# Optimization experiments

Measured on AMD Instinct MI355X. Metric: run time of the kernel, lower is better.

Reference implementation:

```python
import jax, jax.numpy as jnp
import numpy as np

C_EM, H_EM, C_A = 256, 8, 32
S, R = 1024, 256
LN_EPS = 1e-5
MASK_BIAS = 1e9


def setup_inputs() -> dict:
    key = jax.random.key(0)
    ks = jax.random.split(key, 8)
    sc = 0.02
    m = jax.random.normal(ks[0], (S, R, C_EM), jnp.float32)
    # binary column mask (float mask in the original; int here so it is a constant)
    mask = (jax.random.uniform(ks[1], (S, R)) < 0.9).astype(jnp.int32)
    return {
        "m": m,
        "ln_g": jnp.ones((C_EM,), jnp.float32),
        "ln_b": jnp.zeros((C_EM,), jnp.float32),
        "w_q": jax.random.normal(ks[2], (C_EM, H_EM, C_A), jnp.float32) * sc,
        "w_k": jax.random.normal(ks[3], (C_EM, C_A), jnp.float32) * sc,
        "w_v": jax.random.normal(ks[4], (C_EM, C_A), jnp.float32) * sc,
        "w_g": jax.random.normal(ks[5], (C_EM, H_EM, C_A), jnp.float32) * sc,
        "b_g": jnp.zeros((H_EM, C_A), jnp.float32),
        "w_o": jax.random.normal(ks[6], (H_EM, C_A, C_EM), jnp.float32) * sc,
        "b_o": jnp.zeros((C_EM,), jnp.float32),
        "mask": mask,
    }


def reference(m, ln_g, ln_b, w_q, w_k, w_v, w_g, b_g, w_o, b_o, mask):
    maskf = mask.astype(m.dtype)  # [s, r]
    # LayerNorm over c_em (biased variance, eps=1e-5, torch default)
    mu = jnp.mean(m, axis=-1, keepdims=True)
    var = jnp.mean((m - mu) ** 2, axis=-1, keepdims=True)
    x = (m - mu) * jax.lax.rsqrt(var + LN_EPS) * ln_g + ln_b  # [s, r, c]
    # masked mean-pool over s -> per-column query
    q_pool = jnp.sum(x * maskf[..., None], axis=-3) / (jnp.sum(maskf, axis=-2)[..., None] + 1e-10)  # [r, c]
    Q = jnp.einsum('rc,chd->rhd', q_pool, w_q) * (1.0 / np.sqrt(C_A))  # [r, h, d]
    K = jnp.einsum('src,cd->srd', x, w_k)  # [s, r, d]
    V = jnp.einsum('src,cd->srd', x, w_v)  # [s, r, d]
    G = jax.nn.sigmoid(jnp.einsum('src,chd->srhd', x, w_g) + b_g)  # [s, r, h, d]
    bias = (maskf - 1.0) * MASK_BIAS  # [s, r]
    logits = jnp.einsum('rhd,srd->srh', Q, K) + bias[..., None]  # [s, r, h]
    A = jax.nn.softmax(logits, axis=-3)  # softmax over s
    O = jnp.einsum('srh,srd->rhd', A, V)  # [r, h, d]
    out = jnp.einsum('srhd,hdc->src', O[None, :, :, :] * G, w_o) + b_o  # [s, r, c]
    return out
```

## Files before the change

### kernel.cpp

```cpp
#include <hip/hip_runtime.h>
#include <math.h>

#define S_DIM 1024
#define R_DIM 256
#define C_DIM 256
#define SCALE 0.17677669529663687f

typedef short bf16x8 __attribute__((ext_vector_type(8)));
typedef float f32x4 __attribute__((ext_vector_type(4)));

__device__ __forceinline__ float wred(float v) {
#pragma unroll
  for (int m = 32; m >= 1; m >>= 1) v += __shfl_xor(v, m, 64);
  return v;
}

__device__ __forceinline__ short f2bf(float f) {
  union { float f; unsigned u; } v;
  v.f = f;
  unsigned r = v.u + 0x7fffu + ((v.u >> 16) & 1u);
  return (short)(r >> 16);
}

__device__ __forceinline__ float bf2f(short s) {
  union { unsigned u; float f; } v;
  v.u = ((unsigned)(unsigned short)s) << 16;
  return v.f;
}

__device__ __forceinline__ float fast_sigmoid_mul(float o, float gl) {
  return o * __builtin_amdgcn_rcpf(1.f + __expf(-gl));
}

__global__ __launch_bounds__(256)
void k0_prep(const float* __restrict__ w_g, const float* __restrict__ w_o,
             const float* __restrict__ w_k, const float* __restrict__ w_v,
             short* __restrict__ wgB, short* __restrict__ woB,
             short* __restrict__ wkvB) {
  const int id = blockIdx.x * 256 + threadIdx.x;
  if (id < 16384) {
    const int which = id >> 13;
    const int s = id & 8191;
    const int n = s & 255, g = (s >> 8) & 3, kb = s >> 10;
    const float* W = which ? w_o : w_g;
    short* Out = which ? woB : wgB;
#pragma unroll
    for (int j = 0; j < 8; ++j)
      Out[(((size_t)kb * 256 + n) * 4 + g) * 8 + j] =
          f2bf(W[(size_t)(kb * 32 + g * 8 + j) * 256 + n]);
  } else {
    const int s = id - 16384;
    const int n = s & 63, g = (s >> 6) & 3, kb = s >> 8;
    const float* W = (n < 32) ? w_k : w_v;
    const int nn = n & 31;
#pragma unroll
    for (int j = 0; j < 8; ++j)
      wkvB[(((size_t)kb * 64 + n) * 4 + g) * 8 + j] =
          f2bf(W[(size_t)(kb * 32 + g * 8 + j) * 32 + nn]);
  }
}

__global__ __launch_bounds__(256, 3)
void k1_ln_kv(const float* __restrict__ mIn, const float* __restrict__ ln_g,
              const float* __restrict__ ln_b, const short* __restrict__ wkvB,
              const int* __restrict__ mask,
              float* __restrict__ mu_ws, float* __restrict__ rs_ws,
              short* __restrict__ Kt, short* __restrict__ Vt,
              float* __restrict__ pool_ws) {
  __shared__ __align__(16) short A_lds[2048 * 8];
  __shared__ float mask_s[64];
  __shared__ float4 poolp[4][64];
  const int r  = blockIdx.y;
  const int s0 = blockIdx.x * 64;
  const int t  = threadIdx.x;

  if (t < 64) mask_s[t] = mask[(s0 + t) * R_DIM + r] ? 1.f : 0.f;

  {
    const int rw = t >> 2;
    const int q  = t & 3;
    const size_t p = (size_t)(s0 + rw) * R_DIM + r;
    const float* src = mIn + p * C_DIM + q * 64;
    float4 xv[16];
    float sum = 0.f, ssq = 0.f;
#pragma unroll
    for (int i = 0; i < 16; ++i) {
      xv[i] = *(const float4*)(src + i * 4);
      sum += xv[i].x + xv[i].y + xv[i].z + xv[i].w;
      ssq += xv[i].x * xv[i].x + xv[i].y * xv[i].y + xv[i].z * xv[i].z +
             xv[i].w * xv[i].w;
    }
    sum += __shfl_xor(sum, 1, 64); ssq += __shfl_xor(ssq, 1, 64);
    sum += __shfl_xor(sum, 2, 64); ssq += __shfl_xor(ssq, 2, 64);
    const float mu = sum * (1.f / 256.f);
    const float var = ssq * (1.f / 256.f) - mu * mu;
    const float rs = rsqrtf(var + 1e-5f);
    if (q == 0) { mu_ws[p] = mu; rs_ws[p] = rs; }

    const int gw = rw >> 4;
    const int lf0 = rw & 15;
#pragma unroll
    for (int kh = 0; kh < 2; ++kh) {
      const int kb = 2 * q + kh;
#pragma unroll
      for (int g = 0; g < 4; ++g) {
        const int lidx = kh * 32 + g * 8;
        const float4 a0 = xv[lidx >> 2], a1 = xv[(lidx >> 2) + 1];
        const float4 g0 = *(const float4*)(ln_g + kb * 32 + g * 8);
        const float4 g1 = *(const float4*)(ln_g + kb * 32 + g * 8 + 4);
        const float4 b0 = *(const float4*)(ln_b + kb * 32 + g * 8);
        const float4 b1 = *(const float4*)(ln_b + kb * 32 + g * 8 + 4);
        bf16x8 f;
        f[0] = f2bf((a0.x - mu) * rs * g0.x + b0.x);
        f[1] = f2bf((a0.y - mu) * rs * g0.y + b0.y);
        f[2] = f2bf((a0.z - mu) * rs * g0.z + b0.z);
        f[3] = f2bf((a0.w - mu) * rs * g0.w + b0.w);
        f[4] = f2bf((a1.x - mu) * rs * g1.x + b1.x);
        f[5] = f2bf((a1.y - mu) * rs * g1.y + b1.y);
        f[6] = f2bf((a1.z - mu) * rs * g1.z + b1.z);
        f[7] = f2bf((a1.w - mu) * rs * g1.w + b1.w);
        int byte = (((gw * 8 + kb) * 64 + lf0 + g * 16) << 4) ^ (((kb >> 1) & 3) << 5);
        *(bf16x8*)((char*)A_lds + byte) = f;
      }
    }
  }
  __syncthreads();

  {
    const int w = t >> 6, l = t & 63;
    const int lm = l & 15, g = l >> 4;
    f32x4 acc[4];
#pragma unroll
    for (int ni = 0; ni < 4; ++ni) acc[ni] = (f32x4){0.f, 0.f, 0.f, 0.f};
#pragma unroll
    for (int kb = 0; kb < 8; ++kb) {
      const int byte = (((w * 8 + kb) * 64 + l) << 4) ^ (((kb >> 1) & 3) << 5);
      const bf16x8 a = *(const bf16x8*)((char*)A_lds + byte);
      bf16x8 bfr[4];
#pragma unroll
      for (int ni = 0; ni < 4; ++ni)
        bfr[ni] = *(const bf16x8*)(wkvB + (((size_t)kb * 64 + lm + ni * 16) * 4 + g) * 8);
#pragma unroll
      for (int ni = 0; ni < 4; ++ni)
        acc[ni] = __builtin_amdgcn_mfma_f32_16x16x32_bf16(a, bfr[ni], acc[ni], 0, 0, 0);
    }
#pragma unroll
    for (int ni = 0; ni < 4; ++ni) {
      const int col = lm + ni * 16;
      short* Out = (col < 32) ? Kt : Vt;
      const int cc = col & 31;
#pragma unroll
      for (int reg = 0; reg < 4; ++reg) {
        const int s = s0 + w * 16 + g * 4 + reg;
        Out[((size_t)r * 1024 + s) * 32 + cc] = f2bf(acc[ni][reg]);
      }
    }
  }

  {
    const int lc = t & 63;
    const int wq = t >> 6;
    const int kb = lc >> 3, g2 = (lc >> 1) & 3, bh = (lc & 1) * 4;
    float4 ps = make_float4(0.f, 0.f, 0.f, 0.f);
    for (int i = 0; i < 16; ++i) {
      const int rloc = (i + lc) & 15;
      const int byte =
          ((((wq * 8 + kb) * 64 + rloc + g2 * 16) << 4) + bh * 2) ^ (((kb >> 1) & 3) << 5);
      const short4 xb = *(const short4*)((char*)A_lds + byte);
      const float mk = mask_s[wq * 16 + rloc];
      ps.x += mk * bf2f(xb.x);
      ps.y += mk * bf2f(xb.y);
      ps.z += mk * bf2f(xb.z);
      ps.w += mk * bf2f(xb.w);
    }
    poolp[wq][lc] = ps;
  }
  __syncthreads();
  if (t < 64) {
    const float4 a = poolp[0][t], b = poolp[1][t], c = poolp[2][t], d = poolp[3][t];
    atomicAdd(&pool_ws[r * C_DIM + t * 4 + 0], a.x + b.x + c.x + d.x);
    atomicAdd(&pool_ws[r * C_DIM + t * 4 + 1], a.y + b.y + c.y + d.y);
    atomicAdd(&pool_ws[r * C_DIM + t * 4 + 2], a.z + b.z + c.z + d.z);
    atomicAdd(&pool_ws[r * C_DIM + t * 4 + 3], a.w + b.w + c.w + d.w);
  }
}

__global__ __launch_bounds__(256, 2)
void k2_q(const float* __restrict__ pool_ws, const int* __restrict__ mask,
          const float* __restrict__ w_q, float* __restrict__ Q_ws) {
  __shared__ float qp[256];
  __shared__ float wsum[4];
  const int r = blockIdx.x, t = threadIdx.x;
  int cnt = 0;
  for (int s = t; s < S_DIM; s += 256) cnt += mask[s * R_DIM + r];
  float cf = wred((float)cnt);
  if ((t & 63) == 0) wsum[t >> 6] = cf;
  __syncthreads();
  const float denom = wsum[0] + wsum[1] + wsum[2] + wsum[3] + 1e-10f;
  qp[t] = pool_ws[r * C_DIM + t] / denom;
  __syncthreads();
  float acc = 0.f;
  for (int c = 0; c < 256; ++c) acc += qp[c] * w_q[c * 256 + t];
  Q_ws[r * 256 + t] = acc * SCALE;
}

__global__ __launch_bounds__(256, 4)
void k3e_logits(const short* __restrict__ Kt, const float* __restrict__ Q_ws,
                const int* __restrict__ mask, float* __restrict__ E_ws,
                float* __restrict__ D_ws) {
  __shared__ float q[256];
  const int r = blockIdx.y, s0 = blockIdx.x * 64;
  const int t = threadIdx.x, w = t >> 6, l = t & 63;
  q[t] = Q_ws[r * 256 + t];
  __syncthreads();
  const int s = s0 + l;
  const short* kp = Kt + ((size_t)r * 1024 + s) * 32;
  bf16x8 kr[4];
#pragma unroll
  for (int i = 0; i < 4; ++i) kr[i] = *(const bf16x8*)(kp + i * 8);
  const int mk = mask[s * R_DIM + r];
  float e01[2];
#pragma unroll
  for (int hh = 0; hh < 2; ++hh) {
    const int h = 2 * w + hh;
    float a = 0.f;
#pragma unroll
    for (int i = 0; i < 4; ++i)
#pragma unroll
      for (int j = 0; j < 8; ++j)
        a += q[h * 32 + i * 8 + j] * bf2f(kr[i][j]);
    e01[hh] = mk ? __expf(a) : 0.f;
    E_ws[((size_t)r * 8 + h) * 1024 + s] = e01[hh];
  }
  const float d0 = wred(e01[0]);
  const float d1 = wred(e01[1]);
  if (l == 0) {
    atomicAdd(&D_ws[r * 8 + 2 * w + 0], d0);
    atomicAdd(&D_ws[r * 8 + 2 * w + 1], d1);
  }
}

__global__ __launch_bounds__(256, 4)
void k3b_av(const short* __restrict__ Vt, const float* __restrict__ E_ws,
            float* __restrict__ Npart) {
  __shared__ float A_s[8 * 256];
  __shared__ __align__(16) short V_s[256 * 32];
  const int ch = blockIdx.x, r = blockIdx.y;
  const int t = threadIdx.x;
  const int sb = ch * 256;
#pragma unroll
  for (int h = 0; h < 8; ++h)
    A_s[h * 256 + t] = E_ws[((size_t)r * 8 + h) * 1024 + sb + t];
  {
    const short* vp = Vt + ((size_t)r * 1024 + sb) * 32;
#pragma unroll
    for (int i = 0; i < 4; ++i) {
      const int u = i * 256 + t;
      *(bf16x8*)(V_s + u * 8) = *(const bf16x8*)(vp + u * 8);
    }
  }
  __syncthreads();
  const int h = t >> 5, d = t & 31;
  const float* ap = A_s + h * 256;
  float o = 0.f;
  for (int s4 = 0; s4 < 256; s4 += 4) {
    const float4 a4 = *(const float4*)(ap + s4);
    o += a4.x * bf2f(V_s[(s4 + 0) * 32 + d]);
    o += a4.y * bf2f(V_s[(s4 + 1) * 32 + d]);
    o += a4.z * bf2f(V_s[(s4 + 2) * 32 + d]);
    o += a4.w * bf2f(V_s[(s4 + 3) * 32 + d]);
  }
  Npart[(size_t)ch * 65536 + r * 256 + t] = o;
}

__global__ __launch_bounds__(256)
void k3c_norm(const float* __restrict__ Npart, const float* __restrict__ D_ws,
              float* __restrict__ O_ws) {
  const int r = blockIdx.x, t = threadIdx.x;
  const int idx = r * 256 + t;
  const float n = Npart[idx] + Npart[65536 + idx] + Npart[131072 + idx] +
                  Npart[196608 + idx];
  O_ws[idx] = n / (D_ws[r * 8 + (t >> 5)] + 1e-30f);
}

__global__ __launch_bounds__(256, 4)
void k4_mfma(const float* __restrict__ mIn, const float* __restrict__ ln_g,
             const float* __restrict__ ln_b, const float* __restrict__ mu_ws,
             const float* __restrict__ rs_ws, const short* __restrict__ wgB,
             const float* __restrict__ b_g, const float* __restrict__ O_ws,
             const short* __restrict__ woB, const float* __restrict__ b_o,
             float* __restrict__ out) {
  __shared__ __align__(16) short A_lds[2048 * 8];
  const int t = threadIdx.x;
  const int p0 = blockIdx.x * 64;
  const int r0 = p0 & 255;
  const int l = t & 63;
  const int w = t >> 6;
  const int lm = l & 15;
  const int g = l >> 4;

  {
    const int row = w * 16 + lm;
    const size_t p = (size_t)(p0 + row);
    const float mu = mu_ws[p], rs = rs_ws[p];
    const float* mrow = mIn + p * 256 + g * 8;
    const float* gp = ln_g + g * 8;
    const float* bp = ln_b + g * 8;
#pragma unroll
    for (int kb = 0; kb < 8; ++kb) {
      const float4 m0 = *(const float4*)(mrow + kb * 32);
      const float4 m1 = *(const float4*)(mrow + kb * 32 + 4);
      const float4 g0 = *(const float4*)(gp + kb * 32);
      const float4 g1 = *(const float4*)(gp + kb * 32 + 4);
      const float4 b0 = *(const float4*)(bp + kb * 32);
      const float4 b1 = *(const float4*)(bp + kb * 32 + 4);
      bf16x8 xf;
      xf[0] = f2bf((m0.x - mu) * rs * g0.x + b0.x);
      xf[1] = f2bf((m0.y - mu) * rs * g0.y + b0.y);
      xf[2] = f2bf((m0.z - mu) * rs * g0.z + b0.z);
      xf[3] = f2bf((m0.w - mu) * rs * g0.w + b0.w);
      xf[4] = f2bf((m1.x - mu) * rs * g1.x + b1.x);
      xf[5] = f2bf((m1.y - mu) * rs * g1.y + b1.y);
      xf[6] = f2bf((m1.z - mu) * rs * g1.z + b1.z);
      xf[7] = f2bf((m1.w - mu) * rs * g1.w + b1.w);
      *(bf16x8*)(A_lds + ((w * 8 + kb) * 64 + l) * 8) = xf;
    }
  }
  __syncthreads();

  const int col = w * 64 + lm;
  f32x4 acc[4][4];

#pragma unroll
  for (int ni = 0; ni < 4; ++ni) {
    const float bg = b_g[col + ni * 16];
#pragma unroll
    for (int mi = 0; mi < 4; ++mi) acc[mi][ni] = (f32x4){bg, bg, bg, bg};
  }
#pragma unroll
  for (int kb = 0; kb < 8; ++kb) {
    bf16x8 a[4], bb[4];
#pragma unroll
    for (int mi = 0; mi < 4; ++mi)
      a[mi] = *(const bf16x8*)(A_lds + ((mi * 8 + kb) * 64 + l) * 8);
#pragma unroll
    for (int ni = 0; ni < 4; ++ni)
      bb[ni] = *(const bf16x8*)(wgB + (((size_t)kb * 256 + col + ni * 16) * 4 + g) * 8);
#pragma unroll
    for (int mi = 0; mi < 4; ++mi)
#pragma unroll
      for (int ni = 0; ni < 4; ++ni)
        acc[mi][ni] = __builtin_amdgcn_mfma_f32_16x16x32_bf16(a[mi], bb[ni], acc[mi][ni], 0, 0, 0);
  }
  __syncthreads();

#pragma unroll
  for (int mi = 0; mi < 4; ++mi) {
#pragma unroll
    for (int ni = 0; ni < 4; ++ni) {
      const int c2 = col + ni * 16;
      const int kb2 = c2 >> 5, g2 = (c2 >> 3) & 3, b2 = c2 & 7;
#pragma unroll
      for (int reg = 0; reg < 4; ++reg) {
        const int row = mi * 16 + g * 4 + reg;
        const float o = O_ws[(r0 + row) * 256 + c2];
        const float tv = fast_sigmoid_mul(o, acc[mi][ni][reg]);
        const int u = (mi * 8 + kb2) * 64 + (g * 4 + reg) + g2 * 16;
        const int byte = ((u << 4) ^ (((u >> 4) & 3) << 4)) + b2 * 2;
        *(short*)((char*)A_lds + byte) = f2bf(tv);
      }
    }
  }
  __syncthreads();

#pragma unroll
  for (int ni = 0; ni < 4; ++ni) {
    const float bo = b_o[col + ni * 16];
#pragma unroll
    for (int mi = 0; mi < 4; ++mi) acc[mi][ni] = (f32x4){bo, bo, bo, bo};
  }
#pragma unroll
  for (int kb = 0; kb < 8; ++kb) {
    bf16x8 a[4], bb[4];
#pragma unroll
    for (int mi = 0; mi < 4; ++mi) {
      const int u = (mi * 8 + kb) * 64 + l;
      const int byte = (u << 4) ^ (g << 4);
      a[mi] = *(const bf16x8*)((char*)A_lds + byte);
    }
#pragma unroll
    for (int ni = 0; ni < 4; ++ni)
      bb[ni] = *(const bf16x8*)(woB + (((size_t)kb * 256 + col + ni * 16) * 4 + g) * 8);
#pragma unroll
    for (int mi = 0; mi < 4; ++mi)
#pragma unroll
      for (int ni = 0; ni < 4; ++ni)
        acc[mi][ni] = __builtin_amdgcn_mfma_f32_16x16x32_bf16(a[mi], bb[ni], acc[mi][ni], 0, 0, 0);
  }

#pragma unroll
  for (int mi = 0; mi < 4; ++mi)
#pragma unroll
    for (int ni = 0; ni < 4; ++ni)
#pragma unroll
      for (int reg = 0; reg < 4; ++reg) {
        const int row = mi * 16 + g * 4 + reg;
        out[(size_t)(p0 + row) * 256 + col + ni * 16] = acc[mi][ni][reg];
      }
}

extern "C" void kernel_launch(void* const* d_in, const int* in_sizes, int n_in,
                              void* d_out, int out_size, void* d_ws, size_t ws_size,
                              hipStream_t stream) {
  const float* mIn  = (const float*)d_in[0];
  const float* ln_g = (const float*)d_in[1];
  const float* ln_b = (const float*)d_in[2];
  const float* w_q  = (const float*)d_in[3];
  const float* w_k  = (const float*)d_in[4];
  const float* w_v  = (const float*)d_in[5];
  const float* w_g  = (const float*)d_in[6];
  const float* b_g  = (const float*)d_in[7];
  const float* w_o  = (const float*)d_in[8];
  const float* b_o  = (const float*)d_in[9];
  const int*   mask = (const int*)d_in[10];
  float* outp = (float*)d_out;

  float* ws = (float*)d_ws;
  const size_t NP = (size_t)S_DIM * R_DIM;
  float* mu_ws   = ws;
  float* rs_ws   = mu_ws + NP;
  short* Kt      = (short*)(rs_ws + NP);
  short* Vt      = Kt + (size_t)256 * 1024 * 32;
  float* pool_ws = (float*)(Vt + (size_t)256 * 1024 * 32);
  float* D_ws    = pool_ws + 65536;
  float* Q_ws    = D_ws + 2048;
  float* E_ws    = Q_ws + 65536;
  float* Npart   = E_ws + 2097152;
  float* O_ws    = Npart + 262144;
  short* wgB     = (short*)(O_ws + 65536);
  short* woB     = wgB + 65536;
  short* wkvB    = woB + 65536;

  hipMemsetAsync(pool_ws, 0, (65536 + 2048) * sizeof(float), stream);

  k0_prep<<<72, 256, 0, stream>>>(w_g, w_o, w_k, w_v, wgB, woB, wkvB);
  k1_ln_kv<<<dim3(S_DIM / 64, R_DIM), 256, 0, stream>>>(
      mIn, ln_g, ln_b, wkvB, mask, mu_ws, rs_ws, Kt, Vt, pool_ws);
  k2_q<<<R_DIM, 256, 0, stream>>>(pool_ws, mask, w_q, Q_ws);
  k3e_logits<<<dim3(S_DIM / 64, R_DIM), 256, 0, stream>>>(
      Kt, Q_ws, mask, E_ws, D_ws);
  k3b_av<<<dim3(4, R_DIM), 256, 0, stream>>>(Vt, E_ws, Npart);
  k3c_norm<<<R_DIM, 256, 0, stream>>>(Npart, D_ws, O_ws);
  k4_mfma<<<dim3(S_DIM * R_DIM / 64), 256, 0, stream>>>(
      mIn, ln_g, ln_b, mu_ws, rs_ws, wgB, b_g, O_ws, woB, b_o, outp);
}
```

Baseline: 368.3 us.

## Fuse logits and AV kernels, use packed bf16 conversion, raise k1 occupancy

Merges the logits/exp kernel and the attention-value kernel into one, so the exponentiated scores stay in shared memory and the 8 MB E workspace round trip is gone. Each block now also sums its exponentials for the softmax denominator. Separately, the scalar software bf16 rounding is replaced with the hardware v_cvt_pk_bf16_f32 pack instruction in both LN paths, and k1's launch bound goes from 3 to 4 waves. The fused kernel launches only 1024 blocks and keeps 32 K floats per thread in registers, which may cut parallelism. The higher occupancy target could cause register spills.

```diff
diff --git a/kernel.cpp b/kernel.cpp
--- a/kernel.cpp
+++ b/kernel.cpp
@@ -26,6 +26,22 @@
   union { unsigned u; float f; } v;
   v.u = ((unsigned)(unsigned short)s) << 16;
   return v.f;
+}
+
+__device__ __forceinline__ unsigned cvtpk(float lo, float hi) {
+  unsigned r;
+  asm volatile("v_cvt_pk_bf16_f32 %0, %1, %2" : "=v"(r) : "v"(lo), "v"(hi));
+  return r;
+}
+
+__device__ __forceinline__ bf16x8 pack8(float x0, float x1, float x2, float x3,
+                                        float x4, float x5, float x6, float x7) {
+  union { unsigned u[4]; bf16x8 v; } u_;
+  u_.u[0] = cvtpk(x0, x1);
+  u_.u[1] = cvtpk(x2, x3);
+  u_.u[2] = cvtpk(x4, x5);
+  u_.u[3] = cvtpk(x6, x7);
+  return u_.v;
 }
 
 __device__ __forceinline__ float fast_sigmoid_mul(float o, float gl) {
@@ -60,7 +76,7 @@
   }
 }
 
-__global__ __launch_bounds__(256, 3)
+__global__ __launch_bounds__(256, 4)
 void k1_ln_kv(const float* __restrict__ mIn, const float* __restrict__ ln_g,
               const float* __restrict__ ln_b, const short* __restrict__ wkvB,
               const int* __restrict__ mask,
@@ -110,15 +126,11 @@
         const float4 g1 = *(const float4*)(ln_g + kb * 32 + g * 8 + 4);
         const float4 b0 = *(const float4*)(ln_b + kb * 32 + g * 8);
         const float4 b1 = *(const float4*)(ln_b + kb * 32 + g * 8 + 4);
-        bf16x8 f;
-        f[0] = f2bf((a0.x - mu) * rs * g0.x + b0.x);
-        f[1] = f2bf((a0.y - mu) * rs * g0.y + b0.y);
-        f[2] = f2bf((a0.z - mu) * rs * g0.z + b0.z);
-        f[3] = f2bf((a0.w - mu) * rs * g0.w + b0.w);
-        f[4] = f2bf((a1.x - mu) * rs * g1.x + b1.x);
-        f[5] = f2bf((a1.y - mu) * rs * g1.y + b1.y);
-        f[6] = f2bf((a1.z - mu) * rs * g1.z + b1.z);
-        f[7] = f2bf((a1.w - mu) * rs * g1.w + b1.w);
+        const bf16x8 f = pack8(
+            (a0.x - mu) * rs * g0.x + b0.x, (a0.y - mu) * rs * g0.y + b0.y,
+            (a0.z - mu) * rs * g0.z + b0.z, (a0.w - mu) * rs * g0.w + b0.w,
+            (a1.x - mu) * rs * g1.x + b1.x, (a1.y - mu) * rs * g1.y + b1.y,
+            (a1.z - mu) * rs * g1.z + b1.z, (a1.w - mu) * rs * g1.w + b1.w);
         int byte = (((gw * 8 + kb) * 64 + lf0 + g * 16) << 4) ^ (((kb >> 1) & 3) << 5);
         *(bf16x8*)((char*)A_lds + byte) = f;
       }
@@ -205,52 +217,17 @@
 }
 
 __global__ __launch_bounds__(256, 4)
-void k3e_logits(const short* __restrict__ Kt, const float* __restrict__ Q_ws,
-                const int* __restrict__ mask, float* __restrict__ E_ws,
-                float* __restrict__ D_ws) {
+void k3eb(const short* __restrict__ Kt, const short* __restrict__ Vt,
+          const float* __restrict__ Q_ws, const int* __restrict__ mask,
+          float* __restrict__ Npart, float* __restrict__ D_ws) {
   __shared__ float q[256];
-  const int r = blockIdx.y, s0 = blockIdx.x * 64;
-  const int t = threadIdx.x, w = t >> 6, l = t & 63;
-  q[t] = Q_ws[r * 256 + t];
-  __syncthreads();
-  const int s = s0 + l;
-  const short* kp = Kt + ((size_t)r * 1024 + s) * 32;
-  bf16x8 kr[4];
-#pragma unroll
-  for (int i = 0; i < 4; ++i) kr[i] = *(const bf16x8*)(kp + i * 8);
-  const int mk = mask[s * R_DIM + r];
-  float e01[2];
-#pragma unroll
-  for (int hh = 0; hh < 2; ++hh) {
-    const int h = 2 * w + hh;
-    float a = 0.f;
-#pragma unroll
-    for (int i = 0; i < 4; ++i)
-#pragma unroll
-      for (int j = 0; j < 8; ++j)
-        a += q[h * 32 + i * 8 + j] * bf2f(kr[i][j]);
-    e01[hh] = mk ? __expf(a) : 0.f;
-    E_ws[((size_t)r * 8 + h) * 1024 + s] = e01[hh];
-  }
-  const float d0 = wred(e01[0]);
-  const float d1 = wred(e01[1]);
-  if (l == 0) {
-    atomicAdd(&D_ws[r * 8 + 2 * w + 0], d0);
-    atomicAdd(&D_ws[r * 8 + 2 * w + 1], d1);
-  }
-}
-
-__global__ __launch_bounds__(256, 4)
-void k3b_av(const short* __restrict__ Vt, const float* __restrict__ E_ws,
-            float* __restrict__ Npart) {
   __shared__ float A_s[8 * 256];
   __shared__ __align__(16) short V_s[256 * 32];
   const int ch = blockIdx.x, r = blockIdx.y;
   const int t = threadIdx.x;
   const int sb = ch * 256;
-#pragma unroll
-  for (int h = 0; h < 8; ++h)
-    A_s[h * 256 + t] = E_ws[((size_t)r * 8 + h) * 1024 + sb + t];
+
+  q[t] = Q_ws[r * 256 + t];
   {
     const short* vp = Vt + ((size_t)r * 1024 + sb) * 32;
 #pragma unroll
@@ -259,7 +236,28 @@
       *(bf16x8*)(V_s + u * 8) = *(const bf16x8*)(vp + u * 8);
     }
   }
-  __syncthreads();
+  const int s = sb + t;
+  const short* kp = Kt + ((size_t)r * 1024 + s) * 32;
+  bf16x8 kr[4];
+#pragma unroll
+  for (int i = 0; i < 4; ++i) kr[i] = *(const bf16x8*)(kp + i * 8);
+  const int mk = mask[s * R_DIM + r];
+  __syncthreads();
+
+  float kf[32];
+#pragma unroll
+  for (int i = 0; i < 4; ++i)
+#pragma unroll
+    for (int j = 0; j < 8; ++j) kf[i * 8 + j] = bf2f(kr[i][j]);
+#pragma unroll
+  for (int h = 0; h < 8; ++h) {
+    float a = 0.f;
+#pragma unroll
+    for (int d = 0; d < 32; ++d) a += q[h * 32 + d] * kf[d];
+    A_s[h * 256 + t] = mk ? __expf(a) : 0.f;
+  }
+  __syncthreads();
+
   const int h = t >> 5, d = t & 31;
   const float* ap = A_s + h * 256;
   float o = 0.f;
@@ -271,6 +269,11 @@
     o += a4.w * bf2f(V_s[(s4 + 3) * 32 + d]);
   }
   Npart[(size_t)ch * 65536 + r * 256 + t] = o;
+  float ds = 0.f;
+  for (int s1 = d; s1 < 256; s1 += 32) ds += ap[s1];
+#pragma unroll
+  for (int mkk = 16; mkk >= 1; mkk >>= 1) ds += __shfl_xor(ds, mkk, 64);
+  if (d == 0) atomicAdd(&D_ws[r * 8 + h], ds);
 }
 
 __global__ __launch_bounds__(256)
@@ -314,15 +317,11 @@
       const float4 g1 = *(const float4*)(gp + kb * 32 + 4);
       const float4 b0 = *(const float4*)(bp + kb * 32);
       const float4 b1 = *(const float4*)(bp + kb * 32 + 4);
-      bf16x8 xf;
-      xf[0] = f2bf((m0.x - mu) * rs * g0.x + b0.x);
-      xf[1] = f2bf((m0.y - mu) * rs * g0.y + b0.y);
-      xf[2] = f2bf((m0.z - mu) * rs * g0.z + b0.z);
-      xf[3] = f2bf((m0.w - mu) * rs * g0.w + b0.w);
-      xf[4] = f2bf((m1.x - mu) * rs * g1.x + b1.x);
-      xf[5] = f2bf((m1.y - mu) * rs * g1.y + b1.y);
-      xf[6] = f2bf((m1.z - mu) * rs * g1.z + b1.z);
-      xf[7] = f2bf((m1.w - mu) * rs * g1.w + b1.w);
+      const bf16x8 xf = pack8(
+          (m0.x - mu) * rs * g0.x + b0.x, (m0.y - mu) * rs * g0.y + b0.y,
+          (m0.z - mu) * rs * g0.z + b0.z, (m0.w - mu) * rs * g0.w + b0.w,
+          (m1.x - mu) * rs * g1.x + b1.x, (m1.y - mu) * rs * g1.y + b1.y,
+          (m1.z - mu) * rs * g1.z + b1.z, (m1.w - mu) * rs * g1.w + b1.w);
       *(bf16x8*)(A_lds + ((w * 8 + kb) * 64 + l) * 8) = xf;
     }
   }
@@ -434,8 +433,7 @@
   float* pool_ws = (float*)(Vt + (size_t)256 * 1024 * 32);
   float* D_ws    = pool_ws + 65536;
   float* Q_ws    = D_ws + 2048;
-  float* E_ws    = Q_ws + 65536;
-  float* Npart   = E_ws + 2097152;
+  float* Npart   = Q_ws + 65536;
   float* O_ws    = Npart + 262144;
   short* wgB     = (short*)(O_ws + 65536);
   short* woB     = wgB + 65536;
@@ -447,9 +445,7 @@
   k1_ln_kv<<<dim3(S_DIM / 64, R_DIM), 256, 0, stream>>>(
       mIn, ln_g, ln_b, wkvB, mask, mu_ws, rs_ws, Kt, Vt, pool_ws);
   k2_q<<<R_DIM, 256, 0, stream>>>(pool_ws, mask, w_q, Q_ws);
-  k3e_logits<<<dim3(S_DIM / 64, R_DIM), 256, 0, stream>>>(
-      Kt, Q_ws, mask, E_ws, D_ws);
-  k3b_av<<<dim3(4, R_DIM), 256, 0, stream>>>(Vt, E_ws, Npart);
+  k3eb<<<dim3(4, R_DIM), 256, 0, stream>>>(Kt, Vt, Q_ws, mask, Npart, D_ws);
   k3c_norm<<<R_DIM, 256, 0, stream>>>(Npart, D_ws, O_ws);
   k4_mfma<<<dim3(S_DIM * R_DIM / 64), 256, 0, stream>>>(
       mIn, ln_g, ln_b, mu_ws, rs_ws, wgB, b_g, O_ws, woB, b_o, outp);
```

Result: slower. 410.8 us (+11.5%).
